# Kernel optimization log

Hardware: AMD Instinct MI355X
Metric: run time of the kernel (lower is better)

## Reference

```python
import jax, jax.numpy as jnp
import numpy as np
import math

ATTN_C = 32
HEADS = 8
IN_C = 256
PAIR_C = 128
B, M, N = 1, 128, 256


def _layernorm(x, w, b, eps=1e-5):
    mu = jnp.mean(x, axis=-1, keepdims=True)
    xc = x - mu
    var = jnp.mean(xc * xc, axis=-1, keepdims=True)
    return xc * jax.lax.rsqrt(var + eps) * w + b


def setup_inputs() -> dict:
    key = jax.random.key(0)
    ks = jax.random.split(key, 10)
    s1 = 1.0 / math.sqrt(IN_C)
    s2 = 1.0 / math.sqrt(PAIR_C)
    s3 = 1.0 / math.sqrt(ATTN_C * HEADS)
    return {
        "x1d": jax.random.normal(ks[0], (B, M, N, IN_C), jnp.float32),
        "x2d": jax.random.normal(ks[1], (B, N, N, PAIR_C), jnp.float32),
        "norm_w": jnp.ones((IN_C,), jnp.float32),
        "norm_b": jnp.zeros((IN_C,), jnp.float32),
        "qkv_w": jax.random.normal(ks[2], (3 * ATTN_C * HEADS, IN_C), jnp.float32) * s1,
        "x2d_w": jax.random.normal(ks[3], (HEADS, PAIR_C), jnp.float32) * s2,
        "gate_w": jax.random.normal(ks[4], (ATTN_C * HEADS, IN_C), jnp.float32) * s1,
        "gate_b": jnp.zeros((ATTN_C * HEADS,), jnp.float32),
        "final_w": jax.random.normal(ks[5], (IN_C, ATTN_C * HEADS), jnp.float32) * s3,
        "final_b": jnp.zeros((IN_C,), jnp.float32),
    }


def reference(x1d, x2d, norm_w, norm_b, qkv_w, x2d_w, gate_w, gate_b, final_w, final_b):
    c, h = ATTN_C, HEADS
    x = _layernorm(x1d, norm_w, norm_b)                      # [B,M,N,IN_C]
    qkv = (x @ qkv_w.T).reshape(*x.shape[:-1], c, 3 * h)     # [B,M,N,c,3h]
    q, k, v = qkv[..., :h], qkv[..., h:2 * h], qkv[..., 2 * h:]
    aff = jnp.einsum('bmich,bmjch->bmijh', q, k)             # [B,M,N,N,H]
    gate = jax.nn.sigmoid(x @ gate_w.T + gate_b).reshape(*x.shape[:-1], c, h)
    factor = 1.0 / math.sqrt(c)
    bias = (x2d @ x2d_w.T) * factor                          # [B,N,N,H]
    weights = jax.nn.softmax(aff + bias[:, None], axis=-2)   # softmax over j
    out = jnp.einsum('bmrch,bmirh->bmich', v, weights) * gate
    out = out.reshape(*x.shape[:-1], c * h) @ final_w.T + final_b
    return out
```

## Files before the change

### kernel.cpp

```cpp
#include <hip/hip_runtime.h>
#include <math.h>

typedef short bf16x8 __attribute__((ext_vector_type(8)));
typedef float f32x4  __attribute__((ext_vector_type(4)));

#define NPOS 32768

#define OFF_CHI   0u
#define OFF_AHI   100663296u
#define OFF_ATTN  134217728u
#define OFF_BIAST 150994944u
#define OFF_WHI   153354240u
#define OFF_W2P   154402816u
#define OFF_GBP   154533888u

__device__ __forceinline__ short f2bf(float x) {
    unsigned int u = __float_as_uint(x);
    unsigned int r = (u + 0x7FFFu + ((u >> 16) & 1u)) >> 16;
    return (short)r;
}
__device__ __forceinline__ float bf2f(short s) {
    return __uint_as_float(((unsigned int)(unsigned short)s) << 16);
}
__device__ __forceinline__ void async_copy16(const void* g, void* l) {
    __builtin_amdgcn_global_load_lds(
        (const __attribute__((address_space(1))) unsigned int*)g,
        (__attribute__((address_space(3))) unsigned int*)l, 16, 0, 0);
}

__global__ void k_ln_cast(const float* __restrict__ x,
                          const float* __restrict__ nw, const float* __restrict__ nb,
                          short* __restrict__ Ahi) {
    int wid = (blockIdx.x * blockDim.x + threadIdx.x) >> 6;
    int lane = threadIdx.x & 63;
    const float4 v = ((const float4*)(x + (size_t)wid * 256))[lane];
    float s  = v.x + v.y + v.z + v.w;
    float ss = v.x*v.x + v.y*v.y + v.z*v.z + v.w*v.w;
    #pragma unroll
    for (int o = 32; o; o >>= 1) {
        s  += __shfl_xor(s,  o, 64);
        ss += __shfl_xor(ss, o, 64);
    }
    float mu  = s * (1.0f / 256);
    float var = ss * (1.0f / 256) - mu * mu;
    float rs  = rsqrtf(var + 1e-5f);
    const float4 wv = ((const float4*)nw)[lane];
    const float4 bv = ((const float4*)nb)[lane];
    float y[4] = {(v.x - mu) * rs * wv.x + bv.x, (v.y - mu) * rs * wv.y + bv.y,
                  (v.z - mu) * rs * wv.z + bv.z, (v.w - mu) * rs * wv.w + bv.w};
    short h4[4];
    #pragma unroll
    for (int i = 0; i < 4; ++i) h4[i] = f2bf(y[i]);
    *(short4*)(Ahi + (size_t)wid * 256 + lane * 4) = *(short4*)h4;
}

__global__ void k_castw(const float* __restrict__ qkvw, const float* __restrict__ gatew,
                        const float* __restrict__ gateb, const float* __restrict__ finalw,
                        short* __restrict__ Whi, short* __restrict__ W2p,
                        float* __restrict__ gbp) {
    int r = blockIdx.x, t = threadIdx.x;
    if (r < 1024) {
        int which = r >> 8, h = (r >> 5) & 7, c = r & 31;
        const float* src = (which < 3) ? qkvw + (size_t)(c * 24 + which * 8 + h) * 256
                                       : gatew + (size_t)(c * 8 + h) * 256;
        Whi[(size_t)r * 256 + t] = f2bf(src[t]);
    } else if (r < 1280) {
        int o = r - 1024;
        int h = t >> 5, c = t & 31;
        W2p[(size_t)o * 256 + t] = f2bf(finalw[(size_t)o * 256 + c * 8 + h]);
    } else {
        int h = t >> 5, c = t & 31;
        gbp[t] = gateb[c * 8 + h];
    }
}

__global__ __launch_bounds__(256) void k_bias2(const float* __restrict__ x2d,
                                               const float* __restrict__ x2dw,
                                               float* __restrict__ biasT) {
    __shared__ float xs[64][132];
    __shared__ float ws[8][132];
    const int t = threadIdx.x;
    const int wid0 = blockIdx.x * 64;
    #pragma unroll
    for (int r = 0; r < 8; ++r) {
        int g = r * 256 + t;
        int row = g >> 5, c4 = g & 31;
        float4 v = *(const float4*)(x2d + (size_t)(wid0 + row) * 128 + c4 * 4);
        *(float4*)&xs[row][c4 * 4] = v;
    }
    {
        int h = t >> 5, c4 = t & 31;
        *(float4*)&ws[h][c4 * 4] = *(const float4*)(x2dw + h * 128 + c4 * 4);
    }
    __syncthreads();
    const float f = 0.17677669529663687f;
    const int i = wid0 >> 8;
    #pragma unroll
    for (int kk = 0; kk < 2; ++kk) {
        int o = t + kk * 256;
        int row = o >> 3, h = o & 7;
        float acc = 0.f;
        #pragma unroll
        for (int c4 = 0; c4 < 32; ++c4) {
            float4 xv = *(const float4*)&xs[row][c4 * 4];
            float4 wv = *(const float4*)&ws[h][c4 * 4];
            acc += xv.x * wv.x + xv.y * wv.y + xv.z * wv.z + xv.w * wv.w;
        }
        int j = (wid0 & 255) + row;
        biasT[(((h * 256 + j)) << 8) + i] = acc * f;
    }
}

__global__ __launch_bounds__(256) void k_gemm1m(
    const short* __restrict__ Ahi, const short* __restrict__ Whi,
    const float* __restrict__ gbp, short* __restrict__ Chi) {
    __shared__ short As[128 * 64];
    __shared__ short Bs[128 * 64];
    const int t = threadIdx.x;
    const int wave = t >> 6, lane = t & 63, ln15 = lane & 15, quad = lane >> 4;
    const int posBase = blockIdx.x * 128;
    const int nb = blockIdx.y;
    const int i0w = (wave & 1) * 64, n0w = (wave >> 1) * 64;

    f32x4 acc[4][4];
    #pragma unroll
    for (int a = 0; a < 4; ++a)
        #pragma unroll
        for (int b = 0; b < 4; ++b) acc[a][b] = (f32x4){0.f, 0.f, 0.f, 0.f};

    for (int k0 = 0; k0 < 256; k0 += 64) {
        #pragma unroll
        for (int r = 0; r < 4; ++r) {
            int g = r * 256 + t;
            int row = g >> 3, cs = g & 7;
            int colg = cs ^ (row & 7);
            size_t aoff = (size_t)(posBase + row) * 256 + k0 + colg * 8;
            size_t boff = (size_t)(nb * 128 + row) * 256 + k0 + colg * 8;
            int ldst = (r * 256 + wave * 64) * 8;
            async_copy16(Ahi + aoff, &As[ldst]);
            async_copy16(Whi + boff, &Bs[ldst]);
        }
        __syncthreads();
        #pragma unroll
        for (int kc = 0; kc < 2; ++kc) {
            bf16x8 af[4], bfr[4];
            #pragma unroll
            for (int it = 0; it < 4; ++it) {
                int rowa = i0w + it * 16 + ln15;
                int c8a = (kc * 4 + quad) ^ (rowa & 7);
                af[it] = *(const bf16x8*)&As[rowa * 64 + c8a * 8];
                int rowb = n0w + it * 16 + ln15;
                int c8b = (kc * 4 + quad) ^ (rowb & 7);
                bfr[it] = *(const bf16x8*)&Bs[rowb * 64 + c8b * 8];
            }
            #pragma unroll
            for (int it = 0; it < 4; ++it)
                #pragma unroll
                for (int nt = 0; nt < 4; ++nt)
                    acc[it][nt] = __builtin_amdgcn_mfma_f32_16x16x32_bf16(
                        af[it], bfr[nt], acc[it][nt], 0, 0, 0);
        }
        __syncthreads();
    }
    const bool isgate = (nb >= 6);
    #pragma unroll
    for (int it = 0; it < 4; ++it)
        #pragma unroll
        for (int nt = 0; nt < 4; ++nt)
            #pragma unroll
            for (int r = 0; r < 4; ++r) {
                size_t pos = posBase + i0w + it * 16 + quad * 4 + r;
                int ncol = nb * 128 + n0w + nt * 16 + ln15;
                float val = acc[it][nt][r];
                if (isgate) val = 1.0f / (1.0f + __expf(-(val + gbp[ncol - 768])));
                Chi[pos * 1024 + ncol] = f2bf(val);
            }
}

__global__ __launch_bounds__(512) void k_attn3(
    const short* __restrict__ Chi, const float* __restrict__ biasT,
    short* __restrict__ attnB) {
    __shared__ short Khi[256 * 32];
    __shared__ short VT[32 * 264];
    __shared__ short Pl[8][16][40];

    const int mh = blockIdx.x;
    const int m = mh >> 3, h = mh & 7;
    const int t = threadIdx.x;
    const int wave = t >> 6, lane = t & 63, ln15 = lane & 15, quad = lane >> 4;
    const int i0 = wave * 32;

    #pragma unroll
    for (int r = 0; r < 2; ++r) {
        int g = r * 512 + t;
        int j = g >> 2, c16 = g & 3;
        int cs = c16 ^ (j & 3);
        const short* gp = Chi + (size_t)(m * 256 + j) * 1024 + 256 + h * 32 + cs * 8;
        async_copy16(gp, &Khi[(r * 512 + wave * 64) * 8]);
    }
    {
        int j = t & 255, c0 = (t >> 8) * 16;
        const short* vp = Chi + (size_t)(m * 256 + j) * 1024 + 512 + h * 32 + c0;
        bf16x8 v0 = *(const bf16x8*)vp;
        bf16x8 v1 = *(const bf16x8*)(vp + 8);
        #pragma unroll
        for (int c = 0; c < 8; ++c) VT[(c0 + c) * 264 + j] = v0[c];
        #pragma unroll
        for (int c = 0; c < 8; ++c) VT[(c0 + 8 + c) * 264 + j] = v1[c];
    }
    bf16x8 qhi[2];
    #pragma unroll
    for (int it = 0; it < 2; ++it) {
        int i = i0 + it * 16 + ln15;
        qhi[it] = *(const bf16x8*)(Chi + (size_t)(m * 256 + i) * 1024 + h * 32 + quad * 8);
    }
    __syncthreads();

    float lacc[2] = {0.f, 0.f};
    f32x4 Oacc[2][2];
    #pragma unroll
    for (int a = 0; a < 2; ++a) {
        Oacc[a][0] = (f32x4){0.f, 0.f, 0.f, 0.f};
        Oacc[a][1] = (f32x4){0.f, 0.f, 0.f, 0.f};
    }
    const float* bp = biasT + (size_t)h * 65536;

    for (int j0 = 0; j0 < 256; j0 += 32) {
        bf16x8 kfh[2], vf[2];
        #pragma unroll
        for (int jt = 0; jt < 2; ++jt) {
            int j = j0 + jt * 16 + ln15;
            int cs = quad ^ (j & 3);
            kfh[jt] = *(const bf16x8*)&Khi[j * 32 + cs * 8];
        }
        #pragma unroll
        for (int ct = 0; ct < 2; ++ct) {
            int c = ct * 16 + ln15;
            vf[ct] = *(const bf16x8*)&VT[c * 264 + j0 + quad * 8];
        }
        #pragma unroll
        for (int it = 0; it < 2; ++it) {
            int i = i0 + it * 16 + ln15;
            float b0[4], b1[4];
            #pragma unroll
            for (int r = 0; r < 4; ++r) {
                b0[r] = bp[(j0 + quad * 4 + r) * 256 + i];
                b1[r] = bp[(j0 + 16 + quad * 4 + r) * 256 + i];
            }
            f32x4 s0 = (f32x4){0.f, 0.f, 0.f, 0.f};
            f32x4 s1 = (f32x4){0.f, 0.f, 0.f, 0.f};
            s0 = __builtin_amdgcn_mfma_f32_16x16x32_bf16(kfh[0], qhi[it], s0, 0, 0, 0);
            s1 = __builtin_amdgcn_mfma_f32_16x16x32_bf16(kfh[1], qhi[it], s1, 0, 0, 0);
            float p[8], ps = 0.f;
            #pragma unroll
            for (int r = 0; r < 4; ++r) { p[r] = __expf(s0[r] + b0[r]); ps += p[r]; }
            #pragma unroll
            for (int r = 0; r < 4; ++r) { p[4 + r] = __expf(s1[r] + b1[r]); ps += p[4 + r]; }
            lacc[it] += ps;
            unsigned long long pw0 =
                  (unsigned long long)(unsigned short)f2bf(p[0])
                | ((unsigned long long)(unsigned short)f2bf(p[1]) << 16)
                | ((unsigned long long)(unsigned short)f2bf(p[2]) << 32)
                | ((unsigned long long)(unsigned short)f2bf(p[3]) << 48);
            unsigned long long pw1 =
                  (unsigned long long)(unsigned short)f2bf(p[4])
                | ((unsigned long long)(unsigned short)f2bf(p[5]) << 16)
                | ((unsigned long long)(unsigned short)f2bf(p[6]) << 32)
                | ((unsigned long long)(unsigned short)f2bf(p[7]) << 48);
            *(unsigned long long*)&Pl[wave][ln15][quad * 4]      = pw0;
            *(unsigned long long*)&Pl[wave][ln15][16 + quad * 4] = pw1;
            bf16x8 pf = *(const bf16x8*)&Pl[wave][ln15][quad * 8];
            Oacc[it][0] = __builtin_amdgcn_mfma_f32_16x16x32_bf16(pf, vf[0], Oacc[it][0], 0, 0, 0);
            Oacc[it][1] = __builtin_amdgcn_mfma_f32_16x16x32_bf16(pf, vf[1], Oacc[it][1], 0, 0, 0);
        }
    }
    #pragma unroll
    for (int it = 0; it < 2; ++it) {
        float l = lacc[it];
        l += __shfl_xor(l, 16, 64);
        l += __shfl_xor(l, 32, 64);
        float inv = 1.0f / l;
        float invr[4];
        #pragma unroll
        for (int r = 0; r < 4; ++r) invr[r] = __shfl(inv, quad * 4 + r, 16);
        #pragma unroll
        for (int ct = 0; ct < 2; ++ct) {
            int c = ct * 16 + ln15;
            #pragma unroll
            for (int r = 0; r < 4; ++r) {
                int i = i0 + it * 16 + quad * 4 + r;
                float g = bf2f(Chi[(size_t)(m * 256 + i) * 1024 + 768 + h * 32 + c]);
                float val = Oacc[it][ct][r] * invr[r] * g;
                attnB[(size_t)(m * 256 + i) * 256 + h * 32 + c] = f2bf(val);
            }
        }
    }
}

__global__ __launch_bounds__(256) void k_gemm2m(
    const short* __restrict__ A, const short* __restrict__ W2p,
    const float* __restrict__ fb, float* __restrict__ out) {
    __shared__ short As[128 * 64];
    __shared__ short Bs[128 * 64];
    const int t = threadIdx.x;
    const int wave = t >> 6, lane = t & 63, ln15 = lane & 15, quad = lane >> 4;
    const int posBase = blockIdx.x * 128;
    const int nb = blockIdx.y;
    const int i0w = (wave & 1) * 64, n0w = (wave >> 1) * 64;

    f32x4 acc[4][4];
    #pragma unroll
    for (int a = 0; a < 4; ++a)
        #pragma unroll
        for (int b = 0; b < 4; ++b) acc[a][b] = (f32x4){0.f, 0.f, 0.f, 0.f};

    for (int k0 = 0; k0 < 256; k0 += 64) {
        #pragma unroll
        for (int r = 0; r < 4; ++r) {
            int g = r * 256 + t;
            int row = g >> 3, cs = g & 7;
            int colg = cs ^ (row & 7);
            const short* ga = A + (size_t)(posBase + row) * 256 + k0 + colg * 8;
            async_copy16(ga, &As[(r * 256 + wave * 64) * 8]);
            const short* gb = W2p + (size_t)(nb * 128 + row) * 256 + k0 + colg * 8;
            async_copy16(gb, &Bs[(r * 256 + wave * 64) * 8]);
        }
        __syncthreads();
        #pragma unroll
        for (int kc = 0; kc < 2; ++kc) {
            bf16x8 af[4], bfr[4];
            #pragma unroll
            for (int it = 0; it < 4; ++it) {
                int rowa = i0w + it * 16 + ln15;
                int c8a = (kc * 4 + quad) ^ (rowa & 7);
                af[it] = *(const bf16x8*)&As[rowa * 64 + c8a * 8];
                int rowb = n0w + it * 16 + ln15;
                int c8b = (kc * 4 + quad) ^ (rowb & 7);
                bfr[it] = *(const bf16x8*)&Bs[rowb * 64 + c8b * 8];
            }
            #pragma unroll
            for (int it = 0; it < 4; ++it)
                #pragma unroll
                for (int nt = 0; nt < 4; ++nt)
                    acc[it][nt] = __builtin_amdgcn_mfma_f32_16x16x32_bf16(
                        af[it], bfr[nt], acc[it][nt], 0, 0, 0);
        }
        __syncthreads();
    }
    #pragma unroll
    for (int it = 0; it < 4; ++it)
        #pragma unroll
        for (int nt = 0; nt < 4; ++nt)
            #pragma unroll
            for (int r = 0; r < 4; ++r) {
                size_t pos = posBase + i0w + it * 16 + quad * 4 + r;
                int ncol = nb * 128 + n0w + nt * 16 + ln15;
                out[pos * 256 + ncol] = acc[it][nt][r] + fb[ncol];
            }
}

extern "C" void kernel_launch(void* const* d_in, const int* in_sizes, int n_in,
                              void* d_out, int out_size, void* d_ws, size_t ws_size,
                              hipStream_t stream) {
    const float* x1d     = (const float*)d_in[0];
    const float* x2d     = (const float*)d_in[1];
    const float* norm_w  = (const float*)d_in[2];
    const float* norm_b  = (const float*)d_in[3];
    const float* qkv_w   = (const float*)d_in[4];
    const float* x2d_w   = (const float*)d_in[5];
    const float* gate_w  = (const float*)d_in[6];
    const float* gate_b  = (const float*)d_in[7];
    const float* final_w = (const float*)d_in[8];
    const float* final_b = (const float*)d_in[9];
    float* out = (float*)d_out;
    char* w = (char*)d_ws;

    short* Chi   = (short*)(w + OFF_CHI);
    short* Ahi   = (short*)(w + OFF_AHI);
    short* attnB = (short*)(w + OFF_ATTN);
    float* biasT = (float*)(w + OFF_BIAST);
    short* Whi   = (short*)(w + OFF_WHI);
    short* W2p   = (short*)(w + OFF_W2P);
    float* gbp   = (float*)(w + OFF_GBP);

    k_ln_cast<<<NPOS / 4, 256, 0, stream>>>(x1d, norm_w, norm_b, Ahi);
    k_castw<<<1281, 256, 0, stream>>>(qkv_w, gate_w, gate_b, final_w, Whi, W2p, gbp);
    k_bias2<<<1024, 256, 0, stream>>>(x2d, x2d_w, biasT);
    k_gemm1m<<<dim3(256, 8), 256, 0, stream>>>(Ahi, Whi, gbp, Chi);
    k_attn3<<<1024, 512, 0, stream>>>(Chi, biasT, attnB);
    k_gemm2m<<<dim3(256, 2), 256, 0, stream>>>(attnB, W2p, final_b, out);
}
```

Before: 217.7 us.

## Merge prologue kernels into one launch and store bias row-major per i

The layernorm-cast, weight-cast and pair-bias kernels are combined into a single launch that dispatches on block index, removing two launches and the gaps between them. The bias buffer layout changes from [h][j][i] to [h][i][j], so the attention kernel reads its bias with two float4 loads instead of eight strided scalar loads. The bias writes in the prologue become scattered instead, and the shared-memory tiles declared in the bias branch may reduce occupancy for the layernorm blocks.

```diff
diff --git a/kernel.cpp b/kernel.cpp
--- a/kernel.cpp
+++ b/kernel.cpp
@@ -28,86 +28,83 @@
         (__attribute__((address_space(3))) unsigned int*)l, 16, 0, 0);
 }
 
-__global__ void k_ln_cast(const float* __restrict__ x,
-                          const float* __restrict__ nw, const float* __restrict__ nb,
-                          short* __restrict__ Ahi) {
-    int wid = (blockIdx.x * blockDim.x + threadIdx.x) >> 6;
-    int lane = threadIdx.x & 63;
-    const float4 v = ((const float4*)(x + (size_t)wid * 256))[lane];
-    float s  = v.x + v.y + v.z + v.w;
-    float ss = v.x*v.x + v.y*v.y + v.z*v.z + v.w*v.w;
-    #pragma unroll
-    for (int o = 32; o; o >>= 1) {
-        s  += __shfl_xor(s,  o, 64);
-        ss += __shfl_xor(ss, o, 64);
-    }
-    float mu  = s * (1.0f / 256);
-    float var = ss * (1.0f / 256) - mu * mu;
-    float rs  = rsqrtf(var + 1e-5f);
-    const float4 wv = ((const float4*)nw)[lane];
-    const float4 bv = ((const float4*)nb)[lane];
-    float y[4] = {(v.x - mu) * rs * wv.x + bv.x, (v.y - mu) * rs * wv.y + bv.y,
-                  (v.z - mu) * rs * wv.z + bv.z, (v.w - mu) * rs * wv.w + bv.w};
-    short h4[4];
-    #pragma unroll
-    for (int i = 0; i < 4; ++i) h4[i] = f2bf(y[i]);
-    *(short4*)(Ahi + (size_t)wid * 256 + lane * 4) = *(short4*)h4;
-}
-
-__global__ void k_castw(const float* __restrict__ qkvw, const float* __restrict__ gatew,
-                        const float* __restrict__ gateb, const float* __restrict__ finalw,
-                        short* __restrict__ Whi, short* __restrict__ W2p,
-                        float* __restrict__ gbp) {
-    int r = blockIdx.x, t = threadIdx.x;
-    if (r < 1024) {
-        int which = r >> 8, h = (r >> 5) & 7, c = r & 31;
-        const float* src = (which < 3) ? qkvw + (size_t)(c * 24 + which * 8 + h) * 256
-                                       : gatew + (size_t)(c * 8 + h) * 256;
-        Whi[(size_t)r * 256 + t] = f2bf(src[t]);
-    } else if (r < 1280) {
-        int o = r - 1024;
-        int h = t >> 5, c = t & 31;
-        W2p[(size_t)o * 256 + t] = f2bf(finalw[(size_t)o * 256 + c * 8 + h]);
+__global__ __launch_bounds__(256) void k_prologue(
+    const float* __restrict__ x, const float* __restrict__ nw, const float* __restrict__ nbias,
+    const float* __restrict__ qkvw, const float* __restrict__ gatew,
+    const float* __restrict__ gateb, const float* __restrict__ finalw,
+    const float* __restrict__ x2d, const float* __restrict__ x2dw,
+    short* __restrict__ Ahi, short* __restrict__ Whi, short* __restrict__ W2p,
+    float* __restrict__ gbp, float* __restrict__ biasH) {
+    const int b = blockIdx.x, t = threadIdx.x;
+    if (b < 8192) {
+        int wid = (b * 256 + t) >> 6;
+        int lane = t & 63;
+        const float4 v = ((const float4*)(x + (size_t)wid * 256))[lane];
+        float s  = v.x + v.y + v.z + v.w;
+        float ss = v.x*v.x + v.y*v.y + v.z*v.z + v.w*v.w;
+        #pragma unroll
+        for (int o = 32; o; o >>= 1) {
+            s  += __shfl_xor(s,  o, 64);
+            ss += __shfl_xor(ss, o, 64);
+        }
+        float mu  = s * (1.0f / 256);
+        float var = ss * (1.0f / 256) - mu * mu;
+        float rs  = rsqrtf(var + 1e-5f);
+        const float4 wv = ((const float4*)nw)[lane];
+        const float4 bv = ((const float4*)nbias)[lane];
+        float y[4] = {(v.x - mu) * rs * wv.x + bv.x, (v.y - mu) * rs * wv.y + bv.y,
+                      (v.z - mu) * rs * wv.z + bv.z, (v.w - mu) * rs * wv.w + bv.w};
+        short h4[4];
+        #pragma unroll
+        for (int i = 0; i < 4; ++i) h4[i] = f2bf(y[i]);
+        *(short4*)(Ahi + (size_t)wid * 256 + lane * 4) = *(short4*)h4;
+    } else if (b < 9473) {
+        int r = b - 8192;
+        if (r < 1024) {
+            int which = r >> 8, h = (r >> 5) & 7, c = r & 31;
+            const float* src = (which < 3) ? qkvw + (size_t)(c * 24 + which * 8 + h) * 256
+                                           : gatew + (size_t)(c * 8 + h) * 256;
+            Whi[(size_t)r * 256 + t] = f2bf(src[t]);
+        } else if (r < 1280) {
+            int o = r - 1024;
+            int h = t >> 5, c = t & 31;
+            W2p[(size_t)o * 256 + t] = f2bf(finalw[(size_t)o * 256 + c * 8 + h]);
+        } else {
+            int h = t >> 5, c = t & 31;
+            gbp[t] = gateb[c * 8 + h];
+        }
     } else {
-        int h = t >> 5, c = t & 31;
-        gbp[t] = gateb[c * 8 + h];
-    }
-}
-
-__global__ __launch_bounds__(256) void k_bias2(const float* __restrict__ x2d,
-                                               const float* __restrict__ x2dw,
-                                               float* __restrict__ biasT) {
-    __shared__ float xs[64][132];
-    __shared__ float ws[8][132];
-    const int t = threadIdx.x;
-    const int wid0 = blockIdx.x * 64;
-    #pragma unroll
-    for (int r = 0; r < 8; ++r) {
-        int g = r * 256 + t;
-        int row = g >> 5, c4 = g & 31;
-        float4 v = *(const float4*)(x2d + (size_t)(wid0 + row) * 128 + c4 * 4);
-        *(float4*)&xs[row][c4 * 4] = v;
-    }
-    {
-        int h = t >> 5, c4 = t & 31;
-        *(float4*)&ws[h][c4 * 4] = *(const float4*)(x2dw + h * 128 + c4 * 4);
-    }
-    __syncthreads();
-    const float f = 0.17677669529663687f;
-    const int i = wid0 >> 8;
-    #pragma unroll
-    for (int kk = 0; kk < 2; ++kk) {
-        int o = t + kk * 256;
-        int row = o >> 3, h = o & 7;
-        float acc = 0.f;
-        #pragma unroll
-        for (int c4 = 0; c4 < 32; ++c4) {
-            float4 xv = *(const float4*)&xs[row][c4 * 4];
-            float4 wv = *(const float4*)&ws[h][c4 * 4];
-            acc += xv.x * wv.x + xv.y * wv.y + xv.z * wv.z + xv.w * wv.w;
-        }
-        int j = (wid0 & 255) + row;
-        biasT[(((h * 256 + j)) << 8) + i] = acc * f;
+        __shared__ float xs[64][132];
+        __shared__ float ws[8][132];
+        const int wid0 = (b - 9473) * 64;
+        #pragma unroll
+        for (int r = 0; r < 8; ++r) {
+            int g = r * 256 + t;
+            int row = g >> 5, c4 = g & 31;
+            float4 v = *(const float4*)(x2d + (size_t)(wid0 + row) * 128 + c4 * 4);
+            *(float4*)&xs[row][c4 * 4] = v;
+        }
+        {
+            int h = t >> 5, c4 = t & 31;
+            *(float4*)&ws[h][c4 * 4] = *(const float4*)(x2dw + h * 128 + c4 * 4);
+        }
+        __syncthreads();
+        const float f = 0.17677669529663687f;
+        const int i = wid0 >> 8;
+        #pragma unroll
+        for (int kk = 0; kk < 2; ++kk) {
+            int o = t + kk * 256;
+            int row = o >> 3, h = o & 7;
+            float acc = 0.f;
+            #pragma unroll
+            for (int c4 = 0; c4 < 32; ++c4) {
+                float4 xv = *(const float4*)&xs[row][c4 * 4];
+                float4 wv = *(const float4*)&ws[h][c4 * 4];
+                acc += xv.x * wv.x + xv.y * wv.y + xv.z * wv.z + xv.w * wv.w;
+            }
+            int j = (wid0 & 255) + row;
+            biasH[(((h * 256 + i)) << 8) + j] = acc * f;
+        }
     }
 }
 
@@ -178,7 +175,7 @@
 }
 
 __global__ __launch_bounds__(512) void k_attn3(
-    const short* __restrict__ Chi, const float* __restrict__ biasT,
+    const short* __restrict__ Chi, const float* __restrict__ biasH,
     short* __restrict__ attnB) {
     __shared__ short Khi[256 * 32];
     __shared__ short VT[32 * 264];
@@ -223,7 +220,7 @@
         Oacc[a][0] = (f32x4){0.f, 0.f, 0.f, 0.f};
         Oacc[a][1] = (f32x4){0.f, 0.f, 0.f, 0.f};
     }
-    const float* bp = biasT + (size_t)h * 65536;
+    const float* bp = biasH + (size_t)h * 65536;
 
     for (int j0 = 0; j0 < 256; j0 += 32) {
         bf16x8 kfh[2], vf[2];
@@ -241,21 +238,18 @@
         #pragma unroll
         for (int it = 0; it < 2; ++it) {
             int i = i0 + it * 16 + ln15;
-            float b0[4], b1[4];
-            #pragma unroll
-            for (int r = 0; r < 4; ++r) {
-                b0[r] = bp[(j0 + quad * 4 + r) * 256 + i];
-                b1[r] = bp[(j0 + 16 + quad * 4 + r) * 256 + i];
-            }
+            float b0a[4], b1a[4];
+            *(float4*)b0a = *(const float4*)(bp + (size_t)i * 256 + j0 + quad * 4);
+            *(float4*)b1a = *(const float4*)(bp + (size_t)i * 256 + j0 + 16 + quad * 4);
             f32x4 s0 = (f32x4){0.f, 0.f, 0.f, 0.f};
             f32x4 s1 = (f32x4){0.f, 0.f, 0.f, 0.f};
             s0 = __builtin_amdgcn_mfma_f32_16x16x32_bf16(kfh[0], qhi[it], s0, 0, 0, 0);
             s1 = __builtin_amdgcn_mfma_f32_16x16x32_bf16(kfh[1], qhi[it], s1, 0, 0, 0);
             float p[8], ps = 0.f;
             #pragma unroll
-            for (int r = 0; r < 4; ++r) { p[r] = __expf(s0[r] + b0[r]); ps += p[r]; }
-            #pragma unroll
-            for (int r = 0; r < 4; ++r) { p[4 + r] = __expf(s1[r] + b1[r]); ps += p[4 + r]; }
+            for (int r = 0; r < 4; ++r) { p[r] = __expf(s0[r] + b0a[r]); ps += p[r]; }
+            #pragma unroll
+            for (int r = 0; r < 4; ++r) { p[4 + r] = __expf(s1[r] + b1a[r]); ps += p[4 + r]; }
             lacc[it] += ps;
             unsigned long long pw0 =
                   (unsigned long long)(unsigned short)f2bf(p[0])
@@ -378,15 +372,14 @@
     short* Chi   = (short*)(w + OFF_CHI);
     short* Ahi   = (short*)(w + OFF_AHI);
     short* attnB = (short*)(w + OFF_ATTN);
-    float* biasT = (float*)(w + OFF_BIAST);
+    float* biasH = (float*)(w + OFF_BIAST);
     short* Whi   = (short*)(w + OFF_WHI);
     short* W2p   = (short*)(w + OFF_W2P);
     float* gbp   = (float*)(w + OFF_GBP);
 
-    k_ln_cast<<<NPOS / 4, 256, 0, stream>>>(x1d, norm_w, norm_b, Ahi);
-    k_castw<<<1281, 256, 0, stream>>>(qkv_w, gate_w, gate_b, final_w, Whi, W2p, gbp);
-    k_bias2<<<1024, 256, 0, stream>>>(x2d, x2d_w, biasT);
+    k_prologue<<<10497, 256, 0, stream>>>(x1d, norm_w, norm_b, qkv_w, gate_w, gate_b,
+                                          final_w, x2d, x2d_w, Ahi, Whi, W2p, gbp, biasH);
     k_gemm1m<<<dim3(256, 8), 256, 0, stream>>>(Ahi, Whi, gbp, Chi);
-    k_attn3<<<1024, 512, 0, stream>>>(Chi, biasT, attnB);
+    k_attn3<<<1024, 512, 0, stream>>>(Chi, biasH, attnB);
     k_gemm2m<<<dim3(256, 2), 256, 0, stream>>>(attnB, W2p, final_b, out);
 }
```

New measurement: 236.6 us. 8.7% more time.
